# Optimization experiments

Hardware: AMD Instinct MI355X
Metric: run time of the kernel (lower is better)

## Reference

```python
import jax, jax.numpy as jnp
import numpy as np

B, S, H, NH = 4, 2048, 1024, 16
DK = H // NH

def setup_inputs() -> dict:
    key = jax.random.key(0)
    ks = jax.random.split(key, 8)
    query = jax.random.normal(ks[0], (B, S, H), dtype=jnp.float32)
    key_t = jax.random.normal(ks[1], (B, S, H), dtype=jnp.float32)
    value = jax.random.normal(ks[2], (B, S, H), dtype=jnp.float32)
    mask = jnp.ones((B, S), dtype=jnp.int32)
    # Linear weights (torch convention: y = x @ W.T + b)
    sc = 1.0 / np.sqrt(H)
    Wq = jax.random.uniform(ks[3], (H, H), jnp.float32, -sc, sc)
    Wk = jax.random.uniform(ks[4], (H, H), jnp.float32, -sc, sc)
    Wv = jax.random.uniform(ks[5], (H, H), jnp.float32, -sc, sc)
    Wo = jax.random.uniform(ks[6], (H, H), jnp.float32, -sc, sc)
    bo = jax.random.uniform(ks[7], (H,), jnp.float32, -sc, sc)
    return {"query": query, "key": key_t, "value": value, "mask": mask,
            "Wq": Wq, "Wk": Wk, "Wv": Wv, "Wo": Wo, "bo": bo}

def reference(query, key, value, mask, Wq, Wk, Wv, Wo, bo):
    # project and split heads: (B,S,H) -> (B,NH,S,DK)
    def split_heads(x, W):
        y = x @ W.T
        return y.reshape(B, S, NH, DK).transpose(0, 2, 1, 3)
    q = split_heads(query, Wq)
    k = split_heads(key, Wk)
    v = split_heads(value, Wv)
    scores = jnp.einsum('bhqd,bhkd->bhqk', q, k) / jnp.sqrt(jnp.float32(DK))
    # outer-product padding mask: (B,S)x(B,S) -> (B,1,S,S)
    m = (mask[:, :, None] * mask[:, None, :])[:, None, :, :]
    scores = jnp.where(m == 0, jnp.float32(-1e9), scores)
    p = jax.nn.softmax(scores, axis=-1)  # dropout off (eval mode)
    x = jnp.einsum('bhqk,bhkd->bhqd', p, v)
    x = x.transpose(0, 2, 1, 3).reshape(B, S, H)
    return x @ Wo.T + bo
```

## Files before the change

### kernel.cpp

```cpp
#include <hip/hip_runtime.h>

typedef unsigned short u16;
typedef __bf16 bf16x8 __attribute__((ext_vector_type(8)));
typedef __bf16 bf16x4 __attribute__((ext_vector_type(4)));
typedef float f32x4 __attribute__((ext_vector_type(4)));

#if __has_builtin(__builtin_amdgcn_exp2f)
#define EXP2(x) __builtin_amdgcn_exp2f(x)
#else
#define EXP2(x) exp2f(x)
#endif

template<int V> struct IC { static constexpr int val = V; };

__device__ __forceinline__ u16 f2bf(float f) {
    unsigned u = __float_as_uint(f);
    u += 0x7fffu + ((u >> 16) & 1u);
    return (u16)(u >> 16);
}

__device__ __forceinline__ void gll16(const void* g, void* l) {
    __builtin_amdgcn_global_load_lds(
        (const __attribute__((address_space(1))) void*)g,
        (__attribute__((address_space(3))) void*)l, 16, 0, 0);
}

__device__ __forceinline__ void cvt_body(const float* __restrict__ in,
                                         u16* __restrict__ out, int i) {
    float4 v = reinterpret_cast<const float4*>(in)[i];
    unsigned long long pack =
        (unsigned long long)f2bf(v.x) |
        ((unsigned long long)f2bf(v.y) << 16) |
        ((unsigned long long)f2bf(v.z) << 32) |
        ((unsigned long long)f2bf(v.w) << 48);
    reinterpret_cast<unsigned long long*>(out)[i] = pack;
}

__global__ __launch_bounds__(256) void cvt_bf16_3(const float* __restrict__ a,
                                                  const float* __restrict__ b,
                                                  const float* __restrict__ c,
                                                  u16* __restrict__ oa,
                                                  u16* __restrict__ ob,
                                                  u16* __restrict__ oc, int n4) {
    int i = blockIdx.x * 256 + threadIdx.x;
    if (i < n4)            cvt_body(a, oa, i);
    else if (i < 2 * n4)   cvt_body(b, ob, i - n4);
    else if (i < 3 * n4)   cvt_body(c, oc, i - 2 * n4);
}

__global__ __launch_bounds__(256) void cvt_bf16_w(const float* __restrict__ a,
                                                  const float* __restrict__ b,
                                                  const float* __restrict__ c,
                                                  const float* __restrict__ d,
                                                  u16* __restrict__ oa,
                                                  u16* __restrict__ ob,
                                                  u16* __restrict__ oc,
                                                  u16* __restrict__ od, int n4) {
    int i = blockIdx.x * 256 + threadIdx.x;
    if (i < n4)            cvt_body(a, oa, i);
    else if (i < 2 * n4)   cvt_body(b, ob, i - n4);
    else if (i < 3 * n4)   cvt_body(c, oc, i - 2 * n4);
    else if (i < 4 * n4)   cvt_body(d, od, i - 3 * n4);
}

template<int MODE>
__global__ __launch_bounds__(256) void gemm_bt(const u16* __restrict__ A,
                                               const u16* __restrict__ B,
                                               void* __restrict__ Cv,
                                               const float* __restrict__ bias) {
    constexpr int K = 1024, N = 1024;
    __shared__ __align__(16) u16 As[128 * 64];
    __shared__ __align__(16) u16 Bs[128 * 64];
    const int tid = threadIdx.x;
    const int wv = tid >> 6, lane = tid & 63, g = lane >> 4, li = lane & 15;
    const int row0 = blockIdx.y << 7, col0 = blockIdx.x << 7;
    const int wm = wv >> 1, wn = wv & 1;

    f32x4 acc[4][4] = {};

    for (int k0 = 0; k0 < K; k0 += 64) {
        __syncthreads();
#pragma unroll
        for (int i = 0; i < 4; i++) {
            const int o   = (wv << 12) + (i << 10) + (lane << 4);
            const int row = o >> 7;
            const int cbg = (o & 127) ^ ((row & 7) << 4);
            gll16(A + (size_t)(row0 + row) * K + k0 + (cbg >> 1),
                  (char*)As + (wv << 12) + (i << 10));
        }
#pragma unroll
        for (int i = 0; i < 4; i++) {
            const int o   = (wv << 12) + (i << 10) + (lane << 4);
            const int row = o >> 7;
            const int cbg = (o & 127) ^ ((row & 7) << 4);
            gll16(B + (size_t)(col0 + row) * K + k0 + (cbg >> 1),
                  (char*)Bs + (wv << 12) + (i << 10));
        }
        __syncthreads();

#pragma unroll
        for (int kk = 0; kk < 2; kk++) {
            bf16x8 af[4], bfr[4];
            const int cb = ((kk << 5) + (g << 3)) << 1;
#pragma unroll
            for (int m = 0; m < 4; m++) {
                const int row = (wm << 6) + (m << 4) + li;
                af[m] = *reinterpret_cast<const bf16x8*>(
                    (const char*)As + (row << 7) + (cb ^ ((row & 7) << 4)));
            }
#pragma unroll
            for (int n = 0; n < 4; n++) {
                const int row = (wn << 6) + (n << 4) + li;
                bfr[n] = *reinterpret_cast<const bf16x8*>(
                    (const char*)Bs + (row << 7) + (cb ^ ((row & 7) << 4)));
            }
#pragma unroll
            for (int m = 0; m < 4; m++)
#pragma unroll
                for (int n = 0; n < 4; n++)
                    acc[m][n] = __builtin_amdgcn_mfma_f32_16x16x32_bf16(
                        af[m], bfr[n], acc[m][n], 0, 0, 0);
        }
    }

    if constexpr (MODE == 0 || MODE == 3) {
        constexpr float SC = (MODE == 3) ? 0.180336880f : 1.0f;
        u16* C = (u16*)Cv;
#pragma unroll
        for (int m = 0; m < 4; m++)
#pragma unroll
            for (int n = 0; n < 4; n++)
#pragma unroll
                for (int r = 0; r < 4; r++) {
                    int row = row0 + (wm << 6) + (m << 4) + (g << 2) + r;
                    int col = col0 + (wn << 6) + (n << 4) + li;
                    C[(size_t)row * N + col] = f2bf(acc[m][n][r] * SC);
                }
    } else if constexpr (MODE == 1) {
        float* C = (float*)Cv;
#pragma unroll
        for (int m = 0; m < 4; m++)
#pragma unroll
            for (int n = 0; n < 4; n++)
#pragma unroll
                for (int r = 0; r < 4; r++) {
                    int row = row0 + (wm << 6) + (m << 4) + (g << 2) + r;
                    int col = col0 + (wn << 6) + (n << 4) + li;
                    C[(size_t)row * N + col] = acc[m][n][r] + bias[col];
                }
    } else {
        u16* C = (u16*)Cv;
#pragma unroll
        for (int m = 0; m < 4; m++)
#pragma unroll
            for (int n = 0; n < 4; n++) {
                int srow = row0 + (wm << 6) + (m << 4) + (g << 2);
                int col  = col0 + (wn << 6) + (n << 4) + li;
                int b = srow >> 11, s = srow & 2047;
                int nh = col >> 6, d = col & 63;
                unsigned long long pack =
                    (unsigned long long)f2bf(acc[m][n][0]) |
                    ((unsigned long long)f2bf(acc[m][n][1]) << 16) |
                    ((unsigned long long)f2bf(acc[m][n][2]) << 32) |
                    ((unsigned long long)f2bf(acc[m][n][3]) << 48);
                *reinterpret_cast<unsigned long long*>(
                    C + ((size_t)((b << 4) + nh) * 64 + d) * 2048 + s) = pack;
            }
    }
}

__global__ __launch_bounds__(512, 4) void attn_fwd(const u16* __restrict__ Q,
                                                   const u16* __restrict__ Kp,
                                                   const u16* __restrict__ Vt,
                                                   const int* __restrict__ mask,
                                                   u16* __restrict__ O) {
    constexpr int S = 2048, H = 1024;
    __shared__ __align__(16) char lds[32768];
    __shared__ int sm_bad;
    const int tid = threadIdx.x, wv = tid >> 6, lane = tid & 63;
    const int g = lane >> 4, li = lane & 15;
    const int q0 = blockIdx.x << 7, h = blockIdx.y, b = blockIdx.z;
    const char* Kg = (const char*)(Kp + (size_t)b * S * H + h * 64);
    const char* Vg = (const char*)(Vt + (size_t)(b * 16 + h) * 64 * S);

    auto stageKV = [&](int bufOff, int kv2) {
        const int o   = tid << 4;
        const int row = o >> 7;
        const int cbg = (o & 127) ^ ((row & 7) << 4);
        const int gk  = (((row >> 2) & 3) << 4) + ((row >> 4) << 2) + (row & 3);
        gll16(Kg + (size_t)(kv2 + gk) * 2048 + cbg, lds + bufOff + (wv << 10));
        gll16(Vg + (size_t)row * 4096 + kv2 * 2 + cbg, lds + 16384 + bufOff + (wv << 10));
    };

    if (tid == 0) sm_bad = 0;
    stageKV(0, 0);

    bf16x8 qf[2];
    {
        const u16* Qrow = Q + (size_t)(b * S + q0 + (wv << 4) + li) * H + h * 64 + (g << 3);
        qf[0] = *reinterpret_cast<const bf16x8*>(Qrow);
        qf[1] = *reinterpret_cast<const bf16x8*>(Qrow + 32);
    }

    int z = 0;
#pragma unroll
    for (int j = 0; j < 4; j++) z |= (mask[b * S + (tid << 2) + j] == 0);
    __syncthreads();
    if (z) sm_bad = 1;
    __syncthreads();
    const bool bad = (sm_bad != 0);
    const int  mq  = bad ? mask[b * S + q0 + (wv << 4) + li] : 1;

    int offK[2], offV[2];
#pragma unroll
    for (int kk = 0; kk < 2; kk++) {
        offK[kk] = (li << 7) + (((kk << 6) + (g << 4)) ^ ((li & 7) << 4));
        offV[kk] = (li << 7) + (((g << 5) + (kk << 4)) ^ ((li & 7) << 4));
    }

    f32x4 o_[4] = {};
    float l_ = 0.f;

    auto tile = [&](auto BUF, int kv2) {
        constexpr int KOFF = decltype(BUF)::val * 8192;
        constexpr int VOFF = 16384 + decltype(BUF)::val * 8192;
        f32x4 sc[4] = {};
        __builtin_amdgcn_s_setprio(1);
#pragma unroll
        for (int kk = 0; kk < 2; kk++)
#pragma unroll
            for (int n = 0; n < 4; n++) {
                bf16x8 kf = *reinterpret_cast<const bf16x8*>(
                    lds + KOFF + offK[kk] + (n << 11));
                sc[n] = __builtin_amdgcn_mfma_f32_16x16x32_bf16(kf, qf[kk], sc[n], 0, 0, 0);
            }
        __builtin_amdgcn_s_setprio(0);

        if (bad) {
            const unsigned long long kb = __ballot(mask[b * S + kv2 + lane] != 0);
#pragma unroll
            for (int n = 0; n < 4; n++)
#pragma unroll
                for (int r = 0; r < 4; r++) {
                    const int key = (g << 4) + (n << 2) + r;
                    const bool ok = mq && ((kb >> key) & 1ull);
                    sc[n][r] = ok ? sc[n][r] : -1e9f;
                }
        }

        float rs = 0.f;
#pragma unroll
        for (int n = 0; n < 4; n++)
#pragma unroll
            for (int r = 0; r < 4; r++) {
                const float p = EXP2(sc[n][r]);
                sc[n][r] = p;
                rs += p;
            }
        rs += __shfl_xor(rs, 16);
        rs += __shfl_xor(rs, 32);
        l_ += rs;

        bf16x8 pf0, pf1;
#pragma unroll
        for (int j = 0; j < 4; j++) {
            pf0[j]     = (__bf16)sc[0][j];
            pf0[4 + j] = (__bf16)sc[1][j];
            pf1[j]     = (__bf16)sc[2][j];
            pf1[4 + j] = (__bf16)sc[3][j];
        }

        __builtin_amdgcn_s_setprio(1);
#pragma unroll
        for (int kk = 0; kk < 2; kk++) {
            const bf16x8 pf = kk ? pf1 : pf0;
#pragma unroll
            for (int n = 0; n < 4; n++) {
                bf16x8 vf = *reinterpret_cast<const bf16x8*>(
                    lds + VOFF + offV[kk] + (n << 11));
                o_[n] = __builtin_amdgcn_mfma_f32_16x16x32_bf16(pf, vf, o_[n], 0, 0, 0);
            }
        }
        __builtin_amdgcn_s_setprio(0);
    };

    for (int kv = 0; kv < S; kv += 128) {
        stageKV(8192, kv + 64);
        tile(IC<0>{}, kv);
        __syncthreads();
        if (kv + 128 < S) stageKV(0, kv + 128);
        tile(IC<1>{}, kv + 64);
        __syncthreads();
    }

    float linv[4];
#pragma unroll
    for (int r = 0; r < 4; r++) {
        const float lr = __shfl(l_, (lane & 48) + (g << 2) + r);
        linv[r] = lr > 0.f ? 1.f / lr : 0.f;
    }
#pragma unroll
    for (int n = 0; n < 4; n++)
#pragma unroll
        for (int r = 0; r < 4; r++) {
            const int row = q0 + (wv << 4) + (g << 2) + r;
            const int col = (h << 6) + (n << 4) + li;
            O[(size_t)(b * S + row) * H + col] = f2bf(o_[n][r] * linv[r]);
        }
}

extern "C" void kernel_launch(void* const* d_in, const int* in_sizes, int n_in,
                              void* d_out, int out_size, void* d_ws, size_t ws_size,
                              hipStream_t stream) {
    (void)in_sizes; (void)n_in; (void)out_size; (void)ws_size;
    const float* q    = (const float*)d_in[0];
    const float* k    = (const float*)d_in[1];
    const float* v    = (const float*)d_in[2];
    const int*   mask = (const int*)d_in[3];
    const float* Wq   = (const float*)d_in[4];
    const float* Wk   = (const float*)d_in[5];
    const float* Wv   = (const float*)d_in[6];
    const float* Wo   = (const float*)d_in[7];
    const float* bo   = (const float*)d_in[8];

    const size_t NEL = 8192ull * 1024ull;
    u16* ws  = (u16*)d_ws;
    u16* r0  = ws;
    u16* r1  = ws + NEL;
    u16* r2  = ws + 2 * NEL;
    u16* wqb = ws + 3 * NEL;
    u16* wkb = wqb + 1024 * 1024;
    u16* wvb = wkb + 1024 * 1024;
    u16* wob = wvb + 1024 * 1024;
    u16* r4  = wob + 1024 * 1024;

    const int n4 = (int)(NEL / 4);
    const int cvt_blocks = (3 * n4 + 255) / 256;
    cvt_bf16_3<<<dim3(cvt_blocks), dim3(256), 0, stream>>>(q, k, v, r0, r1, r2, n4);
    cvt_bf16_w<<<dim3(4096), dim3(256), 0, stream>>>(Wq, Wk, Wv, Wo,
                                                     wqb, wkb, wvb, wob, 262144);

    dim3 gg(8, 64), bb(256);
    gemm_bt<3><<<gg, bb, 0, stream>>>(r0, wqb, r4, nullptr);
    gemm_bt<0><<<gg, bb, 0, stream>>>(r1, wkb, r0, nullptr);
    gemm_bt<2><<<gg, bb, 0, stream>>>(r2, wvb, r1, nullptr);

    attn_fwd<<<dim3(16, 16, 4), dim3(512), 0, stream>>>(r4, r0, r1, mask, r2);

    gemm_bt<1><<<gg, bb, 0, stream>>>(r2, wob, d_out, bo);
}
```

Before: 218.0 us.

## Halve attention block threads, each wave processes two 16-row query slabs

The attention kernel now runs 256 threads (4 waves) per 128-query block instead of 512, with each wave handling two 16-row query slabs. Every K and V fragment read from LDS is reused across two MFMAs, halving LDS read traffic per MFMA and raising the number of independent MFMAs each wave can issue. Staging loops now issue two loads per thread to fill the same tiles. In exchange, register pressure roughly doubles for the score and accumulator state, and there are fewer waves to hide latency.

```diff
diff --git a/kernel.cpp b/kernel.cpp
--- a/kernel.cpp
+++ b/kernel.cpp
@@ -169,7 +169,7 @@
     }
 }
 
-__global__ __launch_bounds__(512, 4) void attn_fwd(const u16* __restrict__ Q,
+__global__ __launch_bounds__(256, 4) void attn_fwd(const u16* __restrict__ Q,
                                                    const u16* __restrict__ Kp,
                                                    const u16* __restrict__ Vt,
                                                    const int* __restrict__ mask,
@@ -184,32 +184,43 @@
     const char* Vg = (const char*)(Vt + (size_t)(b * 16 + h) * 64 * S);
 
     auto stageKV = [&](int bufOff, int kv2) {
-        const int o   = tid << 4;
-        const int row = o >> 7;
-        const int cbg = (o & 127) ^ ((row & 7) << 4);
-        const int gk  = (((row >> 2) & 3) << 4) + ((row >> 4) << 2) + (row & 3);
-        gll16(Kg + (size_t)(kv2 + gk) * 2048 + cbg, lds + bufOff + (wv << 10));
-        gll16(Vg + (size_t)row * 4096 + kv2 * 2 + cbg, lds + 16384 + bufOff + (wv << 10));
+#pragma unroll
+        for (int i = 0; i < 2; i++) {
+            const int o   = (wv << 11) + (i << 10) + (lane << 4);
+            const int row = o >> 7;
+            const int cbg = (o & 127) ^ ((row & 7) << 4);
+            const int gk  = (((row >> 2) & 3) << 4) + ((row >> 4) << 2) + (row & 3);
+            gll16(Kg + (size_t)(kv2 + gk) * 2048 + cbg,
+                  lds + bufOff + (wv << 11) + (i << 10));
+            gll16(Vg + (size_t)row * 4096 + kv2 * 2 + cbg,
+                  lds + 16384 + bufOff + (wv << 11) + (i << 10));
+        }
     };
 
     if (tid == 0) sm_bad = 0;
     stageKV(0, 0);
 
-    bf16x8 qf[2];
-    {
-        const u16* Qrow = Q + (size_t)(b * S + q0 + (wv << 4) + li) * H + h * 64 + (g << 3);
-        qf[0] = *reinterpret_cast<const bf16x8*>(Qrow);
-        qf[1] = *reinterpret_cast<const bf16x8*>(Qrow + 32);
+    bf16x8 qf[2][2];
+#pragma unroll
+    for (int s = 0; s < 2; s++) {
+        const u16* Qrow = Q + (size_t)(b * S + q0 + (s << 6) + (wv << 4) + li) * H
+                          + h * 64 + (g << 3);
+        qf[s][0] = *reinterpret_cast<const bf16x8*>(Qrow);
+        qf[s][1] = *reinterpret_cast<const bf16x8*>(Qrow + 32);
     }
 
     int z = 0;
 #pragma unroll
-    for (int j = 0; j < 4; j++) z |= (mask[b * S + (tid << 2) + j] == 0);
+    for (int j = 0; j < 8; j++) z |= (mask[b * S + (tid << 3) + j] == 0);
     __syncthreads();
     if (z) sm_bad = 1;
     __syncthreads();
     const bool bad = (sm_bad != 0);
-    const int  mq  = bad ? mask[b * S + q0 + (wv << 4) + li] : 1;
+    int mq[2] = {1, 1};
+    if (bad) {
+        mq[0] = mask[b * S + q0 + (wv << 4) + li];
+        mq[1] = mask[b * S + q0 + 64 + (wv << 4) + li];
+    }
 
     int offK[2], offV[2];
 #pragma unroll
@@ -218,13 +229,13 @@
         offV[kk] = (li << 7) + (((g << 5) + (kk << 4)) ^ ((li & 7) << 4));
     }
 
-    f32x4 o_[4] = {};
-    float l_ = 0.f;
+    f32x4 o_[2][4] = {};
+    float l_[2] = {0.f, 0.f};
 
     auto tile = [&](auto BUF, int kv2) {
         constexpr int KOFF = decltype(BUF)::val * 8192;
         constexpr int VOFF = 16384 + decltype(BUF)::val * 8192;
-        f32x4 sc[4] = {};
+        f32x4 sc[2][4] = {};
         __builtin_amdgcn_s_setprio(1);
 #pragma unroll
         for (int kk = 0; kk < 2; kk++)
@@ -232,55 +243,66 @@
             for (int n = 0; n < 4; n++) {
                 bf16x8 kf = *reinterpret_cast<const bf16x8*>(
                     lds + KOFF + offK[kk] + (n << 11));
-                sc[n] = __builtin_amdgcn_mfma_f32_16x16x32_bf16(kf, qf[kk], sc[n], 0, 0, 0);
+                sc[0][n] = __builtin_amdgcn_mfma_f32_16x16x32_bf16(kf, qf[0][kk],
+                                                                   sc[0][n], 0, 0, 0);
+                sc[1][n] = __builtin_amdgcn_mfma_f32_16x16x32_bf16(kf, qf[1][kk],
+                                                                   sc[1][n], 0, 0, 0);
             }
         __builtin_amdgcn_s_setprio(0);
 
         if (bad) {
             const unsigned long long kb = __ballot(mask[b * S + kv2 + lane] != 0);
 #pragma unroll
+            for (int s = 0; s < 2; s++)
+#pragma unroll
+                for (int n = 0; n < 4; n++)
+#pragma unroll
+                    for (int r = 0; r < 4; r++) {
+                        const int key = (g << 4) + (n << 2) + r;
+                        const bool ok = mq[s] && ((kb >> key) & 1ull);
+                        sc[s][n][r] = ok ? sc[s][n][r] : -1e9f;
+                    }
+        }
+
+#pragma unroll
+        for (int s = 0; s < 2; s++) {
+            float rs = 0.f;
+#pragma unroll
             for (int n = 0; n < 4; n++)
 #pragma unroll
                 for (int r = 0; r < 4; r++) {
-                    const int key = (g << 4) + (n << 2) + r;
-                    const bool ok = mq && ((kb >> key) & 1ull);
-                    sc[n][r] = ok ? sc[n][r] : -1e9f;
+                    const float p = EXP2(sc[s][n][r]);
+                    sc[s][n][r] = p;
+                    rs += p;
                 }
-        }
-
-        float rs = 0.f;
-#pragma unroll
-        for (int n = 0; n < 4; n++)
-#pragma unroll
-            for (int r = 0; r < 4; r++) {
-                const float p = EXP2(sc[n][r]);
-                sc[n][r] = p;
-                rs += p;
-            }
-        rs += __shfl_xor(rs, 16);
-        rs += __shfl_xor(rs, 32);
-        l_ += rs;
-
-        bf16x8 pf0, pf1;
-#pragma unroll
-        for (int j = 0; j < 4; j++) {
-            pf0[j]     = (__bf16)sc[0][j];
-            pf0[4 + j] = (__bf16)sc[1][j];
-            pf1[j]     = (__bf16)sc[2][j];
-            pf1[4 + j] = (__bf16)sc[3][j];
-        }
+            rs += __shfl_xor(rs, 16);
+            rs += __shfl_xor(rs, 32);
+            l_[s] += rs;
+        }
+
+        bf16x8 pf[2][2];
+#pragma unroll
+        for (int s = 0; s < 2; s++)
+#pragma unroll
+            for (int j = 0; j < 4; j++) {
+                pf[s][0][j]     = (__bf16)sc[s][0][j];
+                pf[s][0][4 + j] = (__bf16)sc[s][1][j];
+                pf[s][1][j]     = (__bf16)sc[s][2][j];
+                pf[s][1][4 + j] = (__bf16)sc[s][3][j];
+            }
 
         __builtin_amdgcn_s_setprio(1);
 #pragma unroll
-        for (int kk = 0; kk < 2; kk++) {
-            const bf16x8 pf = kk ? pf1 : pf0;
+        for (int kk = 0; kk < 2; kk++)
 #pragma unroll
             for (int n = 0; n < 4; n++) {
                 bf16x8 vf = *reinterpret_cast<const bf16x8*>(
                     lds + VOFF + offV[kk] + (n << 11));
-                o_[n] = __builtin_amdgcn_mfma_f32_16x16x32_bf16(pf, vf, o_[n], 0, 0, 0);
-            }
-        }
+                o_[0][n] = __builtin_amdgcn_mfma_f32_16x16x32_bf16(pf[0][kk], vf,
+                                                                   o_[0][n], 0, 0, 0);
+                o_[1][n] = __builtin_amdgcn_mfma_f32_16x16x32_bf16(pf[1][kk], vf,
+                                                                   o_[1][n], 0, 0, 0);
+            }
         __builtin_amdgcn_s_setprio(0);
     };
 
@@ -293,20 +315,23 @@
         __syncthreads();
     }
 
-    float linv[4];
-#pragma unroll
-    for (int r = 0; r < 4; r++) {
-        const float lr = __shfl(l_, (lane & 48) + (g << 2) + r);
-        linv[r] = lr > 0.f ? 1.f / lr : 0.f;
-    }
-#pragma unroll
-    for (int n = 0; n < 4; n++)
+#pragma unroll
+    for (int s = 0; s < 2; s++) {
+        float linv[4];
 #pragma unroll
         for (int r = 0; r < 4; r++) {
-            const int row = q0 + (wv << 4) + (g << 2) + r;
-            const int col = (h << 6) + (n << 4) + li;
-            O[(size_t)(b * S + row) * H + col] = f2bf(o_[n][r] * linv[r]);
-        }
+            const float lr = __shfl(l_[s], (lane & 48) + (g << 2) + r);
+            linv[r] = lr > 0.f ? 1.f / lr : 0.f;
+        }
+#pragma unroll
+        for (int n = 0; n < 4; n++)
+#pragma unroll
+            for (int r = 0; r < 4; r++) {
+                const int row = q0 + (s << 6) + (wv << 4) + (g << 2) + r;
+                const int col = (h << 6) + (n << 4) + li;
+                O[(size_t)(b * S + row) * H + col] = f2bf(o_[s][n][r] * linv[r]);
+            }
+    }
 }
 
 extern "C" void kernel_launch(void* const* d_in, const int* in_sizes, int n_in,
@@ -345,7 +370,7 @@
     gemm_bt<0><<<gg, bb, 0, stream>>>(r1, wkb, r0, nullptr);
     gemm_bt<2><<<gg, bb, 0, stream>>>(r2, wvb, r1, nullptr);
 
-    attn_fwd<<<dim3(16, 16, 4), dim3(512), 0, stream>>>(r4, r0, r1, mask, r2);
+    attn_fwd<<<dim3(16, 16, 4), dim3(256), 0, stream>>>(r4, r0, r1, mask, r2);
 
     gemm_bt<1><<<gg, bb, 0, stream>>>(r2, wob, d_out, bo);
 }
```

New measurement: 223.9 us. 1.03x slower.

## Software-pipeline attention QK with softmax/PV across tiles and merge conversion kernels

Applied to the files above, without the earlier changes.

Restructures the attention inner loop so the QK^T product of the next KV tile is computed before the softmax and PV of the current tile. K and V staging are split so their loads can be issued at finer granularity inside the ping-pong buffers. This aims to overlap MFMA work with exp and conversion work and hide LDS load latency, at the cost of more live registers. It also merges the two fp32-to-bf16 conversion kernels into one launch to save a kernel launch.

```diff
diff --git a/kernel.cpp b/kernel.cpp
--- a/kernel.cpp
+++ b/kernel.cpp
@@ -10,8 +10,6 @@
 #else
 #define EXP2(x) exp2f(x)
 #endif
-
-template<int V> struct IC { static constexpr int val = V; };
 
 __device__ __forceinline__ u16 f2bf(float f) {
     unsigned u = __float_as_uint(f);
@@ -36,31 +34,32 @@
     reinterpret_cast<unsigned long long*>(out)[i] = pack;
 }
 
-__global__ __launch_bounds__(256) void cvt_bf16_3(const float* __restrict__ a,
-                                                  const float* __restrict__ b,
-                                                  const float* __restrict__ c,
-                                                  u16* __restrict__ oa,
-                                                  u16* __restrict__ ob,
-                                                  u16* __restrict__ oc, int n4) {
+__global__ __launch_bounds__(256) void cvt_all(const float* __restrict__ q,
+                                               const float* __restrict__ k,
+                                               const float* __restrict__ v,
+                                               const float* __restrict__ wq,
+                                               const float* __restrict__ wk,
+                                               const float* __restrict__ wv,
+                                               const float* __restrict__ wo,
+                                               u16* __restrict__ oq,
+                                               u16* __restrict__ ok,
+                                               u16* __restrict__ ov,
+                                               u16* __restrict__ owq,
+                                               u16* __restrict__ owk,
+                                               u16* __restrict__ owv,
+                                               u16* __restrict__ owo,
+                                               int n4, int nw4) {
     int i = blockIdx.x * 256 + threadIdx.x;
-    if (i < n4)            cvt_body(a, oa, i);
-    else if (i < 2 * n4)   cvt_body(b, ob, i - n4);
-    else if (i < 3 * n4)   cvt_body(c, oc, i - 2 * n4);
-}
-
-__global__ __launch_bounds__(256) void cvt_bf16_w(const float* __restrict__ a,
-                                                  const float* __restrict__ b,
-                                                  const float* __restrict__ c,
-                                                  const float* __restrict__ d,
-                                                  u16* __restrict__ oa,
-                                                  u16* __restrict__ ob,
-                                                  u16* __restrict__ oc,
-                                                  u16* __restrict__ od, int n4) {
-    int i = blockIdx.x * 256 + threadIdx.x;
-    if (i < n4)            cvt_body(a, oa, i);
-    else if (i < 2 * n4)   cvt_body(b, ob, i - n4);
-    else if (i < 3 * n4)   cvt_body(c, oc, i - 2 * n4);
-    else if (i < 4 * n4)   cvt_body(d, od, i - 3 * n4);
+    if (i < n4)          cvt_body(q, oq, i);
+    else if (i < 2 * n4) cvt_body(k, ok, i - n4);
+    else if (i < 3 * n4) cvt_body(v, ov, i - 2 * n4);
+    else {
+        int j = i - 3 * n4;
+        if (j < nw4)          cvt_body(wq, owq, j);
+        else if (j < 2 * nw4) cvt_body(wk, owk, j - nw4);
+        else if (j < 3 * nw4) cvt_body(wv, owv, j - 2 * nw4);
+        else if (j < 4 * nw4) cvt_body(wo, owo, j - 3 * nw4);
+    }
 }
 
 template<int MODE>
@@ -175,6 +174,7 @@
                                                    const int* __restrict__ mask,
                                                    u16* __restrict__ O) {
     constexpr int S = 2048, H = 1024;
+    constexpr int K0OFF = 0, K1OFF = 8192, V0OFF = 16384, V1OFF = 24576;
     __shared__ __align__(16) char lds[32768];
     __shared__ int sm_bad;
     const int tid = threadIdx.x, wv = tid >> 6, lane = tid & 63;
@@ -183,17 +183,24 @@
     const char* Kg = (const char*)(Kp + (size_t)b * S * H + h * 64);
     const char* Vg = (const char*)(Vt + (size_t)(b * 16 + h) * 64 * S);
 
-    auto stageKV = [&](int bufOff, int kv2) {
+    auto stageK = [&](int koff, int kv2) {
         const int o   = tid << 4;
         const int row = o >> 7;
         const int cbg = (o & 127) ^ ((row & 7) << 4);
         const int gk  = (((row >> 2) & 3) << 4) + ((row >> 4) << 2) + (row & 3);
-        gll16(Kg + (size_t)(kv2 + gk) * 2048 + cbg, lds + bufOff + (wv << 10));
-        gll16(Vg + (size_t)row * 4096 + kv2 * 2 + cbg, lds + 16384 + bufOff + (wv << 10));
+        gll16(Kg + (size_t)(kv2 + gk) * 2048 + cbg, lds + koff + (wv << 10));
+    };
+    auto stageV = [&](int voff, int kv2) {
+        const int o   = tid << 4;
+        const int row = o >> 7;
+        const int cbg = (o & 127) ^ ((row & 7) << 4);
+        gll16(Vg + (size_t)row * 4096 + kv2 * 2 + cbg, lds + voff + (wv << 10));
     };
 
     if (tid == 0) sm_bad = 0;
-    stageKV(0, 0);
+    stageK(K0OFF, 0);
+    stageV(V0OFF, 0);
+    stageK(K1OFF, 64);
 
     bf16x8 qf[2];
     {
@@ -207,35 +214,40 @@
     for (int j = 0; j < 4; j++) z |= (mask[b * S + (tid << 2) + j] == 0);
     __syncthreads();
     if (z) sm_bad = 1;
+
+    int offK[2], offV[2];
+#pragma unroll
+    for (int kk = 0; kk < 2; kk++) {
+        offK[kk] = (li << 7) + (((kk << 6) + (g << 4)) ^ ((li & 7) << 4));
+        offV[kk] = (li << 7) + (((g << 5) + (kk << 4)) ^ ((li & 7) << 4));
+    }
+
+    f32x4 scE[4] = {}, scO[4] = {};
+    auto QK = [&](int koff, f32x4 (&sc)[4]) {
+#pragma unroll
+        for (int n = 0; n < 4; n++) sc[n] = f32x4{};
+        __builtin_amdgcn_s_setprio(1);
+#pragma unroll
+        for (int kk = 0; kk < 2; kk++)
+#pragma unroll
+            for (int n = 0; n < 4; n++) {
+                bf16x8 kf = *reinterpret_cast<const bf16x8*>(
+                    lds + koff + offK[kk] + (n << 11));
+                sc[n] = __builtin_amdgcn_mfma_f32_16x16x32_bf16(kf, qf[kk], sc[n], 0, 0, 0);
+            }
+        __builtin_amdgcn_s_setprio(0);
+    };
+
+    QK(K0OFF, scE);
     __syncthreads();
     const bool bad = (sm_bad != 0);
     const int  mq  = bad ? mask[b * S + q0 + (wv << 4) + li] : 1;
 
-    int offK[2], offV[2];
-#pragma unroll
-    for (int kk = 0; kk < 2; kk++) {
-        offK[kk] = (li << 7) + (((kk << 6) + (g << 4)) ^ ((li & 7) << 4));
-        offV[kk] = (li << 7) + (((g << 5) + (kk << 4)) ^ ((li & 7) << 4));
-    }
-
     f32x4 o_[4] = {};
     float l_ = 0.f;
-
-    auto tile = [&](auto BUF, int kv2) {
-        constexpr int KOFF = decltype(BUF)::val * 8192;
-        constexpr int VOFF = 16384 + decltype(BUF)::val * 8192;
-        f32x4 sc[4] = {};
-        __builtin_amdgcn_s_setprio(1);
-#pragma unroll
-        for (int kk = 0; kk < 2; kk++)
-#pragma unroll
-            for (int n = 0; n < 4; n++) {
-                bf16x8 kf = *reinterpret_cast<const bf16x8*>(
-                    lds + KOFF + offK[kk] + (n << 11));
-                sc[n] = __builtin_amdgcn_mfma_f32_16x16x32_bf16(kf, qf[kk], sc[n], 0, 0, 0);
-            }
-        __builtin_amdgcn_s_setprio(0);
-
+    bf16x8 pfE[2], pfO[2];
+
+    auto SM = [&](f32x4 (&sc)[4], bf16x8 (&pf)[2], int kv2) {
         if (bad) {
             const unsigned long long kb = __ballot(mask[b * S + kv2 + lane] != 0);
 #pragma unroll
@@ -247,7 +259,6 @@
                     sc[n][r] = ok ? sc[n][r] : -1e9f;
                 }
         }
-
         float rs = 0.f;
 #pragma unroll
         for (int n = 0; n < 4; n++)
@@ -260,36 +271,42 @@
         rs += __shfl_xor(rs, 16);
         rs += __shfl_xor(rs, 32);
         l_ += rs;
-
-        bf16x8 pf0, pf1;
 #pragma unroll
         for (int j = 0; j < 4; j++) {
-            pf0[j]     = (__bf16)sc[0][j];
-            pf0[4 + j] = (__bf16)sc[1][j];
-            pf1[j]     = (__bf16)sc[2][j];
-            pf1[4 + j] = (__bf16)sc[3][j];
-        }
-
+            pf[0][j]     = (__bf16)sc[0][j];
+            pf[0][4 + j] = (__bf16)sc[1][j];
+            pf[1][j]     = (__bf16)sc[2][j];
+            pf[1][4 + j] = (__bf16)sc[3][j];
+        }
+    };
+
+    auto PV = [&](int voff, bf16x8 (&pf)[2]) {
         __builtin_amdgcn_s_setprio(1);
 #pragma unroll
-        for (int kk = 0; kk < 2; kk++) {
-            const bf16x8 pf = kk ? pf1 : pf0;
+        for (int kk = 0; kk < 2; kk++)
 #pragma unroll
             for (int n = 0; n < 4; n++) {
                 bf16x8 vf = *reinterpret_cast<const bf16x8*>(
-                    lds + VOFF + offV[kk] + (n << 11));
-                o_[n] = __builtin_amdgcn_mfma_f32_16x16x32_bf16(pf, vf, o_[n], 0, 0, 0);
-            }
-        }
+                    lds + voff + offV[kk] + (n << 11));
+                o_[n] = __builtin_amdgcn_mfma_f32_16x16x32_bf16(pf[kk], vf, o_[n], 0, 0, 0);
+            }
         __builtin_amdgcn_s_setprio(0);
     };
 
     for (int kv = 0; kv < S; kv += 128) {
-        stageKV(8192, kv + 64);
-        tile(IC<0>{}, kv);
+        stageV(V1OFF, kv + 64);
+        QK(K1OFF, scO);
+        if (kv + 128 < S) stageK(K0OFF, kv + 128);
+        SM(scE, pfE, kv);
+        PV(V0OFF, pfE);
         __syncthreads();
-        if (kv + 128 < S) stageKV(0, kv + 128);
-        tile(IC<1>{}, kv + 64);
+        if (kv + 128 < S) {
+            stageV(V0OFF, kv + 128);
+            QK(K0OFF, scE);
+        }
+        if (kv + 192 < S) stageK(K1OFF, kv + 192);
+        SM(scO, pfO, kv + 64);
+        PV(V1OFF, pfO);
         __syncthreads();
     }
 
@@ -334,11 +351,11 @@
     u16* wob = wvb + 1024 * 1024;
     u16* r4  = wob + 1024 * 1024;
 
-    const int n4 = (int)(NEL / 4);
-    const int cvt_blocks = (3 * n4 + 255) / 256;
-    cvt_bf16_3<<<dim3(cvt_blocks), dim3(256), 0, stream>>>(q, k, v, r0, r1, r2, n4);
-    cvt_bf16_w<<<dim3(4096), dim3(256), 0, stream>>>(Wq, Wk, Wv, Wo,
-                                                     wqb, wkb, wvb, wob, 262144);
+    const int n4  = (int)(NEL / 4);
+    const int nw4 = 262144;
+    const int cvt_blocks = (3 * n4 + 4 * nw4 + 255) / 256;
+    cvt_all<<<dim3(cvt_blocks), dim3(256), 0, stream>>>(
+        q, k, v, Wq, Wk, Wv, Wo, r0, r1, r2, wqb, wkb, wvb, wob, n4, nw4);
 
     dim3 gg(8, 64), bb(256);
     gemm_bt<3><<<gg, bb, 0, stream>>>(r0, wqb, r4, nullptr);
```

New measurement: 219.1 us. No clear change (+0.5%).
